# Performance work log

Hardware: AMD Instinct MI355X
Metric: run time of the kernel (lower is better)

The kernel has to match this reference:

```python
import jax, jax.numpy as jnp
import numpy as np

EPSILON = 1e-8

def setup_inputs() -> dict:
    key = jax.random.key(0)
    k1, k2, k3, k4 = jax.random.split(key, 4)
    B, C_in, C_out, H, W, S, K = 16, 512, 512, 32, 32, 512, 3
    x = jax.random.normal(k1, (B, C_in, H, W), dtype=jnp.float32)
    w = jax.random.normal(k2, (B, S), dtype=jnp.float32)
    # Linear(style_dim -> in_chan), bias initialized to ones per module code
    style_w = jax.random.normal(k3, (C_in, S), dtype=jnp.float32) * (1.0 / np.sqrt(S))
    style_b = jnp.ones((C_in,), dtype=jnp.float32)
    # kaiming_normal_(fan_in, leaky_relu): std = sqrt(2/(1+0.01^2)) / sqrt(fan_in)
    fan_in = C_in * K * K
    gain = np.sqrt(2.0 / (1.0 + 0.01 ** 2))
    weight = jax.random.normal(k4, (C_out, C_in, K, K), dtype=jnp.float32) * (gain / np.sqrt(fan_in))
    return {"x": x, "w": w, "style_w": style_w, "style_b": style_b, "weight": weight}

def reference(x, w, style_w, style_b, weight):
    B, C, H, W_ = x.shape
    C_out, _, K, _ = weight.shape
    # style modulation: Linear(style_dim -> in_chan)
    style = w @ style_w.T + style_b                       # (B, C_in)
    weights = style[:, None, :, None, None] * weight[None]  # (B, C_out, C_in, K, K)
    # demodulation
    d = jax.lax.rsqrt(jnp.sum(weights * weights, axis=(2, 3, 4), keepdims=True) + EPSILON)
    weights = weights * d
    # grouped conv with groups = batch
    pad = 1 if K > 1 else 0
    xg = x.reshape(1, B * C, H, W_)
    wg = weights.reshape(B * C_out, C, K, K)
    y = jax.lax.conv_general_dilated(
        xg, wg, window_strides=(1, 1), padding=((pad, pad), (pad, pad)),
        dimension_numbers=("NCHW", "OIHW", "NCHW"), feature_group_count=B)
    return y.reshape(B, C_out, H, W_)
```

## Files before the change

kernel.cpp:

```cpp
#include <hip/hip_runtime.h>
#include <hip/hip_bf16.h>

#define NB 16
#define CI 512
#define CO 512
#define HW 1024
#define SD 512
#define EPSI 1e-8f

typedef __attribute__((ext_vector_type(8))) short bf16x8;
typedef __attribute__((ext_vector_type(16))) float f32x16;
typedef __attribute__((ext_vector_type(4))) unsigned int u32x4;

#define GLOAD_LDS16(g, l) __builtin_amdgcn_global_load_lds( \
    (const __attribute__((address_space(1))) unsigned int*)(const void*)(g), \
    (__attribute__((address_space(3))) unsigned int*)(void*)(l), 16, 0, 0)
#define SCHED0() __builtin_amdgcn_sched_barrier(0)
#define SBAR()   __builtin_amdgcn_s_barrier()

__global__ void k_style2(const float* __restrict__ w, const float* __restrict__ sw,
                         const float* __restrict__ sb, float* __restrict__ style) {
    int gw = (blockIdx.x * 256 + threadIdx.x) >> 6;
    int l = threadIdx.x & 63;
    int b = gw >> 9, c = gw & 511;
    const float4* wr = (const float4*)(w + b * SD) + (l << 1);
    const float4* sr = (const float4*)(sw + c * SD) + (l << 1);
    float4 a0 = wr[0], a1 = wr[1], q0 = sr[0], q1 = sr[1];
    float acc = a0.x * q0.x + a0.y * q0.y + a0.z * q0.z + a0.w * q0.w
              + a1.x * q1.x + a1.y * q1.y + a1.z * q1.z + a1.w * q1.w;
#pragma unroll
    for (int off = 32; off > 0; off >>= 1) acc += __shfl_down(acc, off);
    if (l == 0) style[gw] = acc + sb[c];
}

__global__ void k_wprep(const float* __restrict__ wt, float* __restrict__ wsq,
                        __hip_bfloat16* __restrict__ wtb, u32x4* __restrict__ zpage) {
    if (blockIdx.x == 0 && threadIdx.x < 64)
        zpage[threadIdx.x] = (u32x4){0, 0, 0, 0};
    int idx = blockIdx.x * 256 + threadIdx.x;
    const float* p = wt + idx * 9;
    float a = 0.f;
#pragma unroll
    for (int t = 0; t < 9; ++t) {
        float v = p[t];
        a += v * v;
        wtb[t * (CO * CI) + idx] = __float2bfloat16(v);
    }
    wsq[idx] = a;
}

__global__ void k_demod2(const float* __restrict__ style, const float* __restrict__ wsq,
                         float* __restrict__ dv) {
    int gw = (blockIdx.x * 256 + threadIdx.x) >> 6;
    int l = threadIdx.x & 63;
    int b = gw >> 9, co = gw & 511;
    const float4* st = (const float4*)(style + b * CI) + (l << 1);
    const float4* wq = (const float4*)(wsq + co * CI) + (l << 1);
    float4 s0 = st[0], s1 = st[1], q0 = wq[0], q1 = wq[1];
    float acc = s0.x * s0.x * q0.x + s0.y * s0.y * q0.y + s0.z * s0.z * q0.z + s0.w * s0.w * q0.w
              + s1.x * s1.x * q1.x + s1.y * s1.y * q1.y + s1.z * s1.z * q1.z + s1.w * s1.w * q1.w;
#pragma unroll
    for (int off = 32; off > 0; off >>= 1) acc += __shfl_down(acc, off);
    if (l == 0) dv[gw] = rsqrtf(acc + EPSI);
}

__global__ void k_xs(const float* __restrict__ x, const float* __restrict__ style,
                     __hip_bfloat16* __restrict__ xs) {
    __shared__ float tile[32][33];
    int b = blockIdx.z, c0 = blockIdx.y * 32, p0 = blockIdx.x * 32;
    int tx = threadIdx.x & 31, ty = threadIdx.x >> 5;
#pragma unroll
    for (int i = 0; i < 4; ++i) {
        int ci = c0 + ty + i * 8;
        tile[ty + i * 8][tx] = x[(b * CI + ci) * HW + p0 + tx] * style[b * CI + ci];
    }
    __syncthreads();
#pragma unroll
    for (int i = 0; i < 4; ++i) {
        int p = p0 + ty + i * 8;
        xs[(b * HW + p) * CI + c0 + tx] = __float2bfloat16(tile[tx][ty + i * 8]);
    }
}

#define XS_BYTES 26112
#define WBUF_BYTES 16384
#define SMEM_TOTAL (XS_BYTES + 3 * WBUF_BYTES)

extern "C" __global__ __launch_bounds__(256, 2) void k_conv(
        const __hip_bfloat16* __restrict__ wtb,
        const __hip_bfloat16* __restrict__ xs,
        const float* __restrict__ dvec,
        const char* __restrict__ zpage,
        float* __restrict__ out) {
    extern __shared__ char smem[];
    char* Xs  = smem;
    char* Wsb = smem + XS_BYTES;

    const int tid  = threadIdx.x;
    const int lane = tid & 63;
    const int wv   = tid >> 6;
    const int wr   = wv >> 1;
    const int wn   = wv & 1;

    int bid = blockIdx.x;
    int xcd = bid & 7, idx = bid >> 3;
    const int cot = xcd >> 1;
    const int px8 = idx & 7;
    const int b   = (idx >> 3) | ((xcd & 1) << 3);
    const int co0 = cot * 128;
    const int p0  = px8 * 128;
    const int y0  = px8 * 4;

    if (tid < 96) {
        int g = tid & 7;
        int rx = (tid & 8) ? 33 : 0;
        int row = tid >> 4;
        *(u32x4*)(Xs + (row * 34 + rx) * 128 + g * 16) = (u32x4){0, 0, 0, 0};
    }

    const int srcgW = (lane & 7) ^ (lane >> 3);

    auto issueW = [&](int tap, int cin, int bufi) {
        const __hip_bfloat16* wsrc = wtb + ((size_t)tap * CO + co0) * CI + cin;
        char* wdst = Wsb + bufi * WBUF_BYTES;
#pragma unroll
        for (int k = 0; k < 4; ++k) {
            int seg = k * 4 + wv;
            int co_l = seg * 8 + (lane >> 3);
            GLOAD_LDS16(wsrc + co_l * CI + srcgW * 8, wdst + seg * 1024);
        }
    };
    auto issueX = [&](int cin) {
#pragma unroll
        for (int k = 0; k < 6; ++k) {
            int sid = k * 4 + wv;
            int ry = sid >> 2, seg = sid & 3;
            int rx0 = 1 + seg * 8;
            char* ldst = Xs + (ry * 34 + rx0) * 128;
            int y = y0 - 1 + ry;
            int rx = rx0 + (lane >> 3);
            int srcg = (lane & 7) ^ (rx & 7);
            if ((unsigned)y < 32u)
                GLOAD_LDS16(xs + ((size_t)b * HW + (y << 5) + (rx - 1)) * CI + cin + srcg * 8, ldst);
            else
                GLOAD_LDS16(zpage, ldst);
        }
    };

    f32x16 acc[2][2];
#pragma unroll
    for (int m = 0; m < 2; ++m)
#pragma unroll
        for (int n = 0; n < 2; ++n)
            acc[m][n] = (f32x16)(0.f);

    issueW(0, 0, 0);
    issueW(1, 0, 1);
    issueX(0);
    SCHED0();
    asm volatile("s_waitcnt lgkmcnt(0) vmcnt(0)" ::: "memory");
    SCHED0();
    SBAR();
    SCHED0();

    for (int cc = 0; cc < 8; ++cc) {
#pragma unroll
        for (int t = 0; t < 9; ++t) {
            if (!(cc == 7 && t >= 7)) {
                const int tn  = (t <= 6) ? (t + 2) : (t - 7);
                const int cin = ((t <= 6) ? cc : (cc + 1)) * 64;
                issueW(tn, cin, (t + 2) % 3);
            }
            SCHED0();

            const char* Wb = Wsb + (t % 3) * WBUF_BYTES;
            const int ky = t / 3, kx = t - (t / 3) * 3;
            __builtin_amdgcn_s_setprio(1);
#pragma unroll
            for (int q = 0; q < 4; ++q) {
                bf16x8 afr[2], bfr[2];
                int g = (q << 1) + (lane >> 5);
#pragma unroll
                for (int m = 0; m < 2; ++m) {
                    int cr = wr * 64 + m * 32 + (lane & 31);
                    afr[m] = *(const bf16x8*)(Wb + cr * 128 + ((g ^ (cr & 7)) << 4));
                }
#pragma unroll
                for (int n = 0; n < 2; ++n) {
                    int ry = wn * 2 + n + ky;
                    int rx = (lane & 31) + kx;
                    bfr[n] = *(const bf16x8*)(Xs + ((ry * 34 + rx) * 128) +
                                              ((g ^ (rx & 7)) << 4));
                }
#pragma unroll
                for (int m = 0; m < 2; ++m)
#pragma unroll
                    for (int n = 0; n < 2; ++n)
                        acc[m][n] = __builtin_amdgcn_mfma_f32_32x32x16_bf16(afr[m], bfr[n], acc[m][n], 0, 0, 0);
            }
            __builtin_amdgcn_s_setprio(0);

            if (cc == 7 && t == 8) {
            } else if (t == 8) {
                SCHED0();
                asm volatile("s_waitcnt lgkmcnt(0)" ::: "memory");
                SCHED0();
                SBAR();
                SCHED0();
                issueX((cc + 1) * 64);
                SCHED0();
                asm volatile("s_waitcnt lgkmcnt(0) vmcnt(0)" ::: "memory");
                SCHED0();
                SBAR();
                SCHED0();
            } else if (cc == 7 && t == 7) {
                SCHED0();
                asm volatile("s_waitcnt lgkmcnt(0) vmcnt(0)" ::: "memory");
                SCHED0();
                SBAR();
                SCHED0();
            } else {
                SCHED0();
                asm volatile("s_waitcnt lgkmcnt(0) vmcnt(4)" ::: "memory");
                SCHED0();
                SBAR();
                SCHED0();
            }
        }
    }

#pragma unroll
    for (int m = 0; m < 2; ++m) {
#pragma unroll
        for (int r = 0; r < 16; ++r) {
            int co = co0 + wr * 64 + m * 32 + (r & 3) + ((r >> 2) << 3) + ((lane >> 5) << 2);
            float dvv = dvec[b * CO + co];
            float* orow = out + ((size_t)b * CO + co) * HW + p0 + wn * 64;
            orow[lane & 31]        = acc[m][0][r] * dvv;
            orow[32 + (lane & 31)] = acc[m][1][r] * dvv;
        }
    }
}

extern "C" void kernel_launch(void* const* d_in, const int* in_sizes, int n_in,
                              void* d_out, int out_size, void* d_ws, size_t ws_size,
                              hipStream_t stream) {
    const float* x  = (const float*)d_in[0];
    const float* w  = (const float*)d_in[1];
    const float* sw = (const float*)d_in[2];
    const float* sb = (const float*)d_in[3];
    const float* wt = (const float*)d_in[4];
    float* out = (float*)d_out;

    char* ws = (char*)d_ws;
    float* style = (float*)(ws);
    float* dvec  = (float*)(ws + 32768);
    float* wsq   = (float*)(ws + 65536);
    __hip_bfloat16* wtb = (__hip_bfloat16*)(ws + 1114112);
    __hip_bfloat16* xsb = (__hip_bfloat16*)(ws + 5832704);
    char* zpage = ws + 22609920;

    hipFuncSetAttribute((const void*)k_conv,
                        hipFuncAttributeMaxDynamicSharedMemorySize, SMEM_TOTAL);

    k_style2<<<2048, 256, 0, stream>>>(w, sw, sb, style);
    k_wprep<<<1024, 256, 0, stream>>>(wt, wsq, (__hip_bfloat16*)wtb, (u32x4*)zpage);
    k_xs<<<dim3(32, 16, 16), 256, 0, stream>>>(x, style, xsb);
    k_demod2<<<2048, 256, 0, stream>>>(style, wsq, dvec);
    k_conv<<<512, 256, SMEM_TOTAL, stream>>>(wtb, xsb, dvec, zpage, out);
}
```

Before: 99.90 us.

## Restructure conv to 2-wave blocks with double-buffered X tiles and 32-channel steps

The conv kernel now runs 128-thread blocks of two waves. Each wave covers all 128 output channels across 4 M-tiles and 2 pixel rows, so each A fragment is reused across more MFMAs. The input-channel step shrinks from 64 to 32 and the X tile is double-buffered, so the next chunk's X load is issued at tap 0 and overlaps compute. This removes the extra barrier and full drain the old per-chunk X reload needed. In exchange there is less parallelism per block, more accumulator registers, and twice as many outer iterations with smaller LDS tiles.

```diff
diff --git a/kernel.cpp b/kernel.cpp
--- a/kernel.cpp
+++ b/kernel.cpp
@@ -82,11 +82,12 @@
     }
 }
 
-#define XS_BYTES 26112
-#define WBUF_BYTES 16384
-#define SMEM_TOTAL (XS_BYTES + 3 * WBUF_BYTES)
-
-extern "C" __global__ __launch_bounds__(256, 2) void k_conv(
+#define XROW 2176
+#define XS_BYTES (6 * XROW)
+#define WBUF 8192
+#define SMEM_TOTAL (2 * XS_BYTES + 3 * WBUF)
+
+extern "C" __global__ __launch_bounds__(128, 1) void k_conv(
         const __hip_bfloat16* __restrict__ wtb,
         const __hip_bfloat16* __restrict__ xs,
         const float* __restrict__ dvec,
@@ -94,13 +95,12 @@
         float* __restrict__ out) {
     extern __shared__ char smem[];
     char* Xs  = smem;
-    char* Wsb = smem + XS_BYTES;
+    char* Wsb = smem + 2 * XS_BYTES;
 
     const int tid  = threadIdx.x;
     const int lane = tid & 63;
     const int wv   = tid >> 6;
-    const int wr   = wv >> 1;
-    const int wn   = wv & 1;
+    const int wn   = wv;
 
     int bid = blockIdx.x;
     int xcd = bid & 7, idx = bid >> 3;
@@ -112,116 +112,103 @@
     const int y0  = px8 * 4;
 
     if (tid < 96) {
-        int g = tid & 7;
-        int rx = (tid & 8) ? 33 : 0;
-        int row = tid >> 4;
-        *(u32x4*)(Xs + (row * 34 + rx) * 128 + g * 16) = (u32x4){0, 0, 0, 0};
-    }
-
-    const int srcgW = (lane & 7) ^ (lane >> 3);
+        int bufi = tid / 48, r = tid % 48;
+        int ry = r >> 3, c = (r >> 2) & 1, s = r & 3;
+        *(u32x4*)(Xs + bufi * XS_BYTES + ry * XROW + c * (33 * 64) + s * 16) = (u32x4){0,0,0,0};
+    }
+
+    const int l31 = lane & 31;
+    const int baseA = l31 * 64 + (((lane >> 5) ^ (lane & 3)) << 4);
+    int baseB[3];
+#pragma unroll
+    for (int kx = 0; kx < 3; ++kx) {
+        int rx = l31 + kx;
+        baseB[kx] = rx * 64 + (((lane >> 5) ^ (rx & 3)) << 4);
+    }
+    const int gW = (lane & 3) ^ ((lane >> 2) & 3);
 
     auto issueW = [&](int tap, int cin, int bufi) {
         const __hip_bfloat16* wsrc = wtb + ((size_t)tap * CO + co0) * CI + cin;
-        char* wdst = Wsb + bufi * WBUF_BYTES;
+        char* wdst = Wsb + bufi * WBUF;
 #pragma unroll
         for (int k = 0; k < 4; ++k) {
-            int seg = k * 4 + wv;
-            int co_l = seg * 8 + (lane >> 3);
-            GLOAD_LDS16(wsrc + co_l * CI + srcgW * 8, wdst + seg * 1024);
+            int u = k * 2 + wv;
+            int co_l = u * 16 + (lane >> 2);
+            GLOAD_LDS16(wsrc + co_l * CI + gW * 8, wdst + u * 1024);
         }
     };
-    auto issueX = [&](int cin) {
+    auto issueX = [&](char* Xdst, int cin) {
 #pragma unroll
         for (int k = 0; k < 6; ++k) {
-            int sid = k * 4 + wv;
-            int ry = sid >> 2, seg = sid & 3;
-            int rx0 = 1 + seg * 8;
-            char* ldst = Xs + (ry * 34 + rx0) * 128;
+            int u = k * 2 + wv;
+            int ry = u >> 1, half = u & 1;
+            int rx = 1 + half * 16 + (lane >> 2);
+            int g = (lane & 3) ^ (rx & 3);
             int y = y0 - 1 + ry;
-            int rx = rx0 + (lane >> 3);
-            int srcg = (lane & 7) ^ (rx & 7);
+            char* ldst = Xdst + ry * XROW + 64 + half * 1024;
             if ((unsigned)y < 32u)
-                GLOAD_LDS16(xs + ((size_t)b * HW + (y << 5) + (rx - 1)) * CI + cin + srcg * 8, ldst);
+                GLOAD_LDS16(xs + ((size_t)b * HW + (y << 5) + (rx - 1)) * CI + cin + g * 8, ldst);
             else
                 GLOAD_LDS16(zpage, ldst);
         }
     };
 
-    f32x16 acc[2][2];
-#pragma unroll
-    for (int m = 0; m < 2; ++m)
+    f32x16 acc[4][2];
+#pragma unroll
+    for (int m = 0; m < 4; ++m)
 #pragma unroll
         for (int n = 0; n < 2; ++n)
             acc[m][n] = (f32x16)(0.f);
 
     issueW(0, 0, 0);
     issueW(1, 0, 1);
-    issueX(0);
+    issueX(Xs, 0);
     SCHED0();
     asm volatile("s_waitcnt lgkmcnt(0) vmcnt(0)" ::: "memory");
     SCHED0();
     SBAR();
     SCHED0();
 
-    for (int cc = 0; cc < 8; ++cc) {
+    for (int cc = 0; cc < 16; ++cc) {
+        const char* Xc = Xs + (cc & 1) * XS_BYTES;
+        const int cin = cc * 32;
 #pragma unroll
         for (int t = 0; t < 9; ++t) {
-            if (!(cc == 7 && t >= 7)) {
-                const int tn  = (t <= 6) ? (t + 2) : (t - 7);
-                const int cin = ((t <= 6) ? cc : (cc + 1)) * 64;
-                issueW(tn, cin, (t + 2) % 3);
-            }
+            if (t <= 6)            issueW(t + 2, cin, (t + 2) % 3);
+            else if (cc < 15)      issueW(t - 7, cin + 32, (t + 2) % 3);
+            if (t == 0 && cc < 15) issueX(Xs + ((cc + 1) & 1) * XS_BYTES, cin + 32);
             SCHED0();
 
-            const char* Wb = Wsb + (t % 3) * WBUF_BYTES;
+            const char* Wb = Wsb + (t % 3) * WBUF;
             const int ky = t / 3, kx = t - (t / 3) * 3;
             __builtin_amdgcn_s_setprio(1);
 #pragma unroll
-            for (int q = 0; q < 4; ++q) {
-                bf16x8 afr[2], bfr[2];
-                int g = (q << 1) + (lane >> 5);
-#pragma unroll
-                for (int m = 0; m < 2; ++m) {
-                    int cr = wr * 64 + m * 32 + (lane & 31);
-                    afr[m] = *(const bf16x8*)(Wb + cr * 128 + ((g ^ (cr & 7)) << 4));
-                }
-#pragma unroll
-                for (int n = 0; n < 2; ++n) {
-                    int ry = wn * 2 + n + ky;
-                    int rx = (lane & 31) + kx;
-                    bfr[n] = *(const bf16x8*)(Xs + ((ry * 34 + rx) * 128) +
-                                              ((g ^ (rx & 7)) << 4));
-                }
-#pragma unroll
-                for (int m = 0; m < 2; ++m)
+            for (int q = 0; q < 2; ++q) {
+                const int qx = q << 5;
+                bf16x8 afr[4], bfr[2];
+#pragma unroll
+                for (int m = 0; m < 4; ++m)
+                    afr[m] = *(const bf16x8*)(Wb + m * 2048 + (baseA ^ qx));
+#pragma unroll
+                for (int n = 0; n < 2; ++n)
+                    bfr[n] = *(const bf16x8*)(Xc + (wn * 2 + n + ky) * XROW + (baseB[kx] ^ qx));
+#pragma unroll
+                for (int m = 0; m < 4; ++m)
 #pragma unroll
                     for (int n = 0; n < 2; ++n)
                         acc[m][n] = __builtin_amdgcn_mfma_f32_32x32x16_bf16(afr[m], bfr[n], acc[m][n], 0, 0, 0);
             }
             __builtin_amdgcn_s_setprio(0);
 
-            if (cc == 7 && t == 8) {
-            } else if (t == 8) {
+            if (!(cc == 15 && t == 8)) {
                 SCHED0();
-                asm volatile("s_waitcnt lgkmcnt(0)" ::: "memory");
-                SCHED0();
-                SBAR();
-                SCHED0();
-                issueX((cc + 1) * 64);
-                SCHED0();
-                asm volatile("s_waitcnt lgkmcnt(0) vmcnt(0)" ::: "memory");
-                SCHED0();
-                SBAR();
-                SCHED0();
-            } else if (cc == 7 && t == 7) {
-                SCHED0();
-                asm volatile("s_waitcnt lgkmcnt(0) vmcnt(0)" ::: "memory");
-                SCHED0();
-                SBAR();
-                SCHED0();
-            } else {
-                SCHED0();
-                asm volatile("s_waitcnt lgkmcnt(0) vmcnt(4)" ::: "memory");
+                if (cc < 15) {
+                    if (t < 2) asm volatile("s_waitcnt lgkmcnt(0) vmcnt(10)" ::: "memory");
+                    else       asm volatile("s_waitcnt lgkmcnt(0) vmcnt(4)" ::: "memory");
+                } else {
+                    if (t == 7) asm volatile("s_waitcnt lgkmcnt(0) vmcnt(0)" ::: "memory");
+                    else        asm volatile("s_waitcnt lgkmcnt(0) vmcnt(4)" ::: "memory");
+                }
                 SCHED0();
                 SBAR();
                 SCHED0();
@@ -230,14 +217,14 @@
     }
 
 #pragma unroll
-    for (int m = 0; m < 2; ++m) {
+    for (int m = 0; m < 4; ++m) {
 #pragma unroll
         for (int r = 0; r < 16; ++r) {
-            int co = co0 + wr * 64 + m * 32 + (r & 3) + ((r >> 2) << 3) + ((lane >> 5) << 2);
+            int co = co0 + m * 32 + (r & 3) + ((r >> 2) << 3) + ((lane >> 5) << 2);
             float dvv = dvec[b * CO + co];
             float* orow = out + ((size_t)b * CO + co) * HW + p0 + wn * 64;
-            orow[lane & 31]        = acc[m][0][r] * dvv;
-            orow[32 + (lane & 31)] = acc[m][1][r] * dvv;
+            orow[l31]      = acc[m][0][r] * dvv;
+            orow[32 + l31] = acc[m][1][r] * dvv;
         }
     }
 }
@@ -267,5 +254,5 @@
     k_wprep<<<1024, 256, 0, stream>>>(wt, wsq, (__hip_bfloat16*)wtb, (u32x4*)zpage);
     k_xs<<<dim3(32, 16, 16), 256, 0, stream>>>(x, style, xsb);
     k_demod2<<<2048, 256, 0, stream>>>(style, wsq, dvec);
-    k_conv<<<512, 256, SMEM_TOTAL, stream>>>(wtb, xsb, dvec, zpage, out);
-}
+    k_conv<<<512, 128, SMEM_TOTAL, stream>>>(wtb, xsb, dvec, zpage, out);
+}
```

Measured after the change: 121.9 us. +22.0%, slower.
